# Optimization experiments

Hardware: AMD Instinct MI355X
Metric: run time of the kernel (lower is better)

The kernel has to match this reference:

```python
import jax, jax.numpy as jnp
import numpy as np

B, L, D = 4, 2048, 256
EXPAND, D_STATE, D_CONV = 2, 16, 4
D_INNER = EXPAND * D
DT_RANK = (D + 15) // 16  # ceil(d_model/16) = 16
N_HEADS = 4
H_MLP = int(D * 4.0)
EPS = 1e-5


def _ln(x, w, b):
    mu = x.mean(-1, keepdims=True)
    var = ((x - mu) ** 2).mean(-1, keepdims=True)
    return (x - mu) / jnp.sqrt(var + EPS) * w + b


def _silu(x):
    return x * jax.nn.sigmoid(x)


def _mamba(x, Win, convw, convb, Wx, Wdt, bdt, Alog, Dp, Wout):
    # x: (B, L, D) -> (B, L, D). Standard Mamba mixer (selective scan).
    b, l, d = x.shape
    xz = x @ Win.T                      # (b, l, 2*d_inner)
    xi, z = jnp.split(xz, 2, axis=-1)
    # depthwise causal conv1d, kernel D_CONV
    xc = jnp.swapaxes(xi, 1, 2)         # (b, d_inner, l)
    xc = jax.lax.conv_general_dilated(
        xc, convw, (1,), [(D_CONV - 1, 0)],
        feature_group_count=D_INNER, dimension_numbers=('NCW', 'OIW', 'NCW'))
    xi = _silu(jnp.swapaxes(xc + convb[None, :, None], 1, 2))  # (b, l, d_inner)
    dbl = xi @ Wx.T                     # (b, l, dt_rank + 2*d_state)
    dt = jax.nn.softplus(dbl[..., :DT_RANK] @ Wdt.T + bdt)     # (b, l, d_inner)
    Bm = dbl[..., DT_RANK:DT_RANK + D_STATE]                    # (b, l, n)
    Cm = dbl[..., DT_RANK + D_STATE:]                            # (b, l, n)
    A = -jnp.exp(Alog)                  # (d_inner, n)

    def step(h, ins):
        dt_t, B_t, C_t, u_t = ins       # (b,d_inner),(b,n),(b,n),(b,d_inner)
        h = h * jnp.exp(dt_t[..., None] * A) + dt_t[..., None] * B_t[:, None, :] * u_t[..., None]
        return h, jnp.einsum('bdn,bn->bd', h, C_t)

    xs = tuple(jnp.swapaxes(t, 0, 1) for t in (dt, Bm, Cm, xi))  # time-major
    h0 = jnp.zeros((b, D_INNER, D_STATE), x.dtype)
    _, ys = jax.lax.scan(step, h0, xs)  # ys: (l, b, d_inner)
    y = jnp.swapaxes(ys, 0, 1) + xi * Dp
    return (y * _silu(z)) @ Wout.T


def _attn(x, Wqkv, bqkv, Wo, bo):
    b, l, d = x.shape
    hd = d // N_HEADS
    qkv = x @ Wqkv.T + bqkv
    q, k, v = jnp.split(qkv, 3, axis=-1)
    sh = lambda t: t.reshape(b, l, N_HEADS, hd).transpose(0, 2, 1, 3)
    q, k, v = sh(q), sh(k), sh(v)
    a = jax.nn.softmax(jnp.einsum('bhqd,bhkd->bhqk', q, k) / np.float32(np.sqrt(hd)), axis=-1)
    o = jnp.einsum('bhqk,bhkd->bhqd', a, v).transpose(0, 2, 1, 3).reshape(b, l, d)
    return o @ Wo.T + bo


def setup_inputs() -> dict:
    key = jax.random.key(0)
    ks = iter(jax.random.split(key, 40))
    rn = lambda shape, s=0.02: jax.random.normal(next(ks), shape, jnp.float32) * s
    inp = {'x': jax.random.normal(next(ks), (B, L, D), jnp.float32)}
    for p in ('mf', 'mb'):
        inp[p + '_Win'] = rn((2 * D_INNER, D))
        inp[p + '_convw'] = rn((D_INNER, 1, D_CONV), 0.1)
        inp[p + '_convb'] = jnp.zeros((D_INNER,), jnp.float32)
        inp[p + '_Wx'] = rn((DT_RANK + 2 * D_STATE, D_INNER))
        inp[p + '_Wdt'] = rn((D_INNER, DT_RANK), 0.1)
        inp[p + '_bdt'] = rn((D_INNER,), 0.5)
        inp[p + '_Alog'] = jnp.log(jnp.broadcast_to(jnp.arange(1, D_STATE + 1, dtype=jnp.float32), (D_INNER, D_STATE)))
        inp[p + '_D'] = jnp.ones((D_INNER,), jnp.float32)
        inp[p + '_Wout'] = rn((D, D_INNER))
    for n in ('n1', 'n2', 'n3'):
        inp[n + 'w'] = jnp.ones((D,), jnp.float32)
        inp[n + 'b'] = jnp.zeros((D,), jnp.float32)
    inp['Wqkv'] = rn((3 * D, D))
    inp['bqkv'] = jnp.zeros((3 * D,), jnp.float32)
    inp['Wo'] = rn((D, D))
    inp['bo'] = jnp.zeros((D,), jnp.float32)
    inp['fc1w'] = rn((H_MLP, D))
    inp['fc1b'] = jnp.zeros((H_MLP,), jnp.float32)
    inp['fc2w'] = rn((D, H_MLP))
    inp['fc2b'] = jnp.zeros((D,), jnp.float32)
    return inp


def reference(x, n1w, n1b, n2w, n2b, n3w, n3b,
              mf_Win, mf_convw, mf_convb, mf_Wx, mf_Wdt, mf_bdt, mf_Alog, mf_D, mf_Wout,
              mb_Win, mb_convw, mb_convb, mb_Wx, mb_Wdt, mb_bdt, mb_Alog, mb_D, mb_Wout,
              Wqkv, bqkv, Wo, bo, fc1w, fc1b, fc2w, fc2b):
    # Mamba branch (bidirectional): DropPath is identity at eval
    h = _ln(x, n1w, n1b)
    fwd = _mamba(h, mf_Win, mf_convw, mf_convb, mf_Wx, mf_Wdt, mf_bdt, mf_Alog, mf_D, mf_Wout)
    bwd = jnp.flip(_mamba(jnp.flip(h, 1), mb_Win, mb_convw, mb_convb, mb_Wx, mb_Wdt, mb_bdt, mb_Alog, mb_D, mb_Wout), 1)
    x = x + fwd + bwd
    # Attention branch (full attention since window=None)
    x = x + _attn(_ln(x, n2w, n2b), Wqkv, bqkv, Wo, bo)
    # MLP branch (exact GELU like torch default)
    h = _ln(x, n3w, n3b)
    x = x + (jax.nn.gelu(h @ fc1w.T + fc1b, approximate=False) @ fc2w.T + fc2b)
    return x
```

## Files before the change

kernel.cpp:

```cpp
#include <hip/hip_runtime.h>
#include <hip/hip_bf16.h>
#include <math.h>

#define LL 2048
#define DD 256
#define MTOT 8192
#define DINNER 512
#define CT 32
#define NC 64

typedef __attribute__((ext_vector_type(8))) short short8;
typedef __attribute__((ext_vector_type(4))) float f32x4;

__device__ __forceinline__ float us2f(unsigned short u){
  return __uint_as_float(((unsigned)u) << 16);
}
__device__ __forceinline__ unsigned short f2us(float f){
  __hip_bfloat16 h = __float2bfloat16(f);
  return *(unsigned short*)&h;
}
__device__ __forceinline__ float frcp(float x){
  return __builtin_amdgcn_rcpf(x);
}

__global__ void probe_kernel(const unsigned* __restrict__ alog, int* __restrict__ flag){
  if (threadIdx.x == 0 && blockIdx.x == 0) *flag = (alog[0] != 0u) ? 1 : 0;
}

struct Srcs { const void* p[32]; unsigned off[33]; unsigned foff[32]; };

__global__ __launch_bounds__(256) void cvt_all_kernel(Srcs s, float* __restrict__ dst,
                                                      unsigned short* __restrict__ db,
                                                      const int* __restrict__ flag,
                                                      unsigned total){
  unsigned i = blockIdx.x * 256u + threadIdx.x;
  if (i >= total) return;
  int k = 31;
  while (s.off[k] > i) --k;
  unsigned j = i - s.off[k];
  float v;
  if (*flag) v = us2f(((const unsigned short*)s.p[k])[j]);
  else       v = ((const float*)s.p[k])[j];
  if ((k == 24 && j < 65536u) || (k == 25 && j < 256u)) v *= 0.125f;
  db[i] = f2us(v);
  if (s.foff[k] != 0xFFFFFFFFu) dst[s.foff[k] + j] = v;
}

__global__ __launch_bounds__(256) void cvt_x_kernel(const void* __restrict__ src,
                                                    float* __restrict__ dst,
                                                    const int* __restrict__ flag, unsigned n){
  unsigned i = blockIdx.x * 256u + threadIdx.x;
  if (i >= n) return;
  if (*flag) dst[i] = us2f(((const unsigned short*)src)[i]);
  else       dst[i] = ((const float*)src)[i];
}

__global__ __launch_bounds__(256) void zero_kernel(float* __restrict__ p, unsigned n){
  unsigned i = blockIdx.x * 256u + threadIdx.x;
  if (i < n) p[i] = 0.f;
}

__global__ __launch_bounds__(256) void wdbl_prep_kernel(
    const float* __restrict__ Wx, int dsWx, unsigned short* __restrict__ Wd)
{
  const unsigned g = blockIdx.x * 256u + threadIdx.x;
  const int dir = g >> 15;
  const unsigned idx = g & 32767u;
  const int n = idx >> 9, k = idx & 511;
  float v = (n < 48) ? (Wx + (size_t)dir * dsWx)[(size_t)n * 512 + k] : 0.f;
  Wd[g] = f2us(v);
}

__global__ __launch_bounds__(256) void final_out_kernel(
    const float* __restrict__ xf, void* __restrict__ out,
    const int* __restrict__ flag, unsigned n)
{
  unsigned i = blockIdx.x * 256u + threadIdx.x;
  if (i >= n) return;
  float v = xf[i];
  if (*flag) ((unsigned short*)out)[i] = f2us(v);
  else       ((float*)out)[i] = v;
}

enum { G_BF16=0, G_GELU=1, G_RESID=2 };
__global__ __launch_bounds__(256) void gemm_mfma_kernel(
    const unsigned short* __restrict__ A, int lda, int agap,
    const unsigned short* __restrict__ W, const unsigned short* __restrict__ W2,
    int Kw, int nsplit, int ksplit, int msplit,
    const float* __restrict__ bias,
    unsigned short* __restrict__ Cb, float* __restrict__ resid,
    int N, int K, int kslices, int mode)
{
  __shared__ unsigned short sA[64][40];
  __shared__ unsigned short sW[64][40];
  const int tid = threadIdx.x;
  const int w = tid >> 6, lane = tid & 63, quad = lane >> 4, l16 = lane & 15;
  const int m0 = blockIdx.y << 6, n0 = blockIdx.x << 6;
  const int ks = blockIdx.z;
  const int kper = K / kslices;
  const int srow = tid >> 2, skc = (tid & 3) << 3;
  int wr = n0 + srow;
  const unsigned short* Wbase = W;
  if (msplit && m0 >= msplit) Wbase = W2;
  if (nsplit && wr >= nsplit){ Wbase = W2; wr -= nsplit; }
  f32x4 acc[4] = {};
  for (int k0 = ks * kper; k0 < ks * kper + kper; k0 += 32){
    int ac = k0 + skc;
    if (agap && ac >= 512) ac += 512;
    short8 av = *(const short8*)(A + (size_t)(m0 + srow) * lda + ac);
    int kk = k0 + skc;
    const unsigned short* Wp = Wbase;
    if (ksplit && kk >= ksplit){ Wp = W2; kk -= ksplit; }
    short8 wv = *(const short8*)(Wp + (size_t)wr * Kw + kk);
    __syncthreads();
    *(short8*)&sA[srow][skc] = av;
    *(short8*)&sW[srow][skc] = wv;
    __syncthreads();
    short8 af = *(const short8*)&sA[w * 16 + l16][quad << 3];
    #pragma unroll
    for (int ns = 0; ns < 4; ++ns){
      short8 wf = *(const short8*)&sW[ns * 16 + l16][quad << 3];
      acc[ns] = __builtin_amdgcn_mfma_f32_16x16x32_bf16(af, wf, acc[ns], 0, 0, 0);
    }
  }
  #pragma unroll
  for (int ns = 0; ns < 4; ++ns){
    const int n = n0 + ns * 16 + l16;
    const float bv = (bias && (mode != G_RESID || ks == 0)) ? bias[n] : 0.f;
    #pragma unroll
    for (int r = 0; r < 4; ++r){
      const int m = m0 + w * 16 + quad * 4 + r;
      const size_t off = (size_t)m * N + n;
      float v = acc[ns][r] + bv;
      if (mode == G_BF16) Cb[off] = f2us(v);
      else if (mode == G_GELU) Cb[off] = f2us(0.5f * v * (1.f + erff(v * 0.70710678118f)));
      else atomicAdd(resid + off, v);
    }
  }
}

__global__ __launch_bounds__(256) void gemm128_kernel(
    const unsigned short* __restrict__ A, int lda,
    const unsigned short* __restrict__ W, const unsigned short* __restrict__ W2,
    int Kw, int nsplit, const float* __restrict__ bias,
    unsigned short* __restrict__ Cb, int N, int K, int mode)
{
  __shared__ unsigned short sA[128][40];
  __shared__ unsigned short sW[128][40];
  const int tid = threadIdx.x;
  const int w = tid >> 6, lane = tid & 63, quad = lane >> 4, l16 = lane & 15;
  const int wm = (w >> 1) << 6, wn = (w & 1) << 6;
  const int m0 = blockIdx.y << 7, n0 = blockIdx.x << 7;
  const int srow = tid >> 2, skc = (tid & 3) << 3;
  const unsigned short* wrp0;
  const unsigned short* wrp1;
  {
    int r0 = n0 + srow, r1 = n0 + srow + 64;
    const unsigned short* b0 = W;
    const unsigned short* b1 = W;
    if (nsplit){
      if (r0 >= nsplit){ b0 = W2; r0 -= nsplit; }
      if (r1 >= nsplit){ b1 = W2; r1 -= nsplit; }
    }
    wrp0 = b0 + (size_t)r0 * Kw;
    wrp1 = b1 + (size_t)r1 * Kw;
  }
  const unsigned short* arp0 = A + (size_t)(m0 + srow) * lda;
  const unsigned short* arp1 = A + (size_t)(m0 + srow + 64) * lda;
  f32x4 acc[4][4] = {};
  for (int k0 = 0; k0 < K; k0 += 32){
    short8 av0 = *(const short8*)(arp0 + k0 + skc);
    short8 av1 = *(const short8*)(arp1 + k0 + skc);
    short8 wv0 = *(const short8*)(wrp0 + k0 + skc);
    short8 wv1 = *(const short8*)(wrp1 + k0 + skc);
    __syncthreads();
    *(short8*)&sA[srow][skc] = av0;
    *(short8*)&sA[srow + 64][skc] = av1;
    *(short8*)&sW[srow][skc] = wv0;
    *(short8*)&sW[srow + 64][skc] = wv1;
    __syncthreads();
    short8 af[4], wf[4];
    #pragma unroll
    for (int i = 0; i < 4; ++i){
      af[i] = *(const short8*)&sA[wm + i * 16 + l16][quad << 3];
      wf[i] = *(const short8*)&sW[wn + i * 16 + l16][quad << 3];
    }
    #pragma unroll
    for (int mi = 0; mi < 4; ++mi)
      #pragma unroll
      for (int ni = 0; ni < 4; ++ni)
        acc[mi][ni] = __builtin_amdgcn_mfma_f32_16x16x32_bf16(af[mi], wf[ni], acc[mi][ni], 0, 0, 0);
  }
  #pragma unroll
  for (int ni = 0; ni < 4; ++ni){
    const int n = n0 + wn + ni * 16 + l16;
    const float bv = bias ? bias[n] : 0.f;
    #pragma unroll
    for (int mi = 0; mi < 4; ++mi){
      #pragma unroll
      for (int r = 0; r < 4; ++r){
        const int m = m0 + wm + mi * 16 + quad * 4 + r;
        float v = acc[mi][ni][r] + bv;
        if (mode == G_GELU) v = 0.5f * v * (1.f + erff(v * 0.70710678118f));
        Cb[(size_t)m * N + n] = f2us(v);
      }
    }
  }
}

__global__ __launch_bounds__(256) void ln_kernel(
    const float* __restrict__ xin,
    const float* __restrict__ w, const float* __restrict__ b,
    unsigned short* __restrict__ hout)
{
  const int row = blockIdx.x, tid = threadIdx.x;
  const size_t off = (size_t)row * DD + tid;
  float v = xin[off];
  float s = v, s2 = v * v;
  #pragma unroll
  for (int o = 32; o; o >>= 1){ s += __shfl_xor(s, o); s2 += __shfl_xor(s2, o); }
  __shared__ float ls[4], ls2[4];
  if ((tid & 63) == 0){ ls[tid >> 6] = s; ls2[tid >> 6] = s2; }
  __syncthreads();
  s  = ls[0] + ls[1] + ls[2] + ls[3];
  s2 = ls2[0] + ls2[1] + ls2[2] + ls2[3];
  const float mu  = s * (1.f / DD);
  const float var = s2 * (1.f / DD) - mu * mu;
  const float inv = rsqrtf(var + 1e-5f);
  hout[off] = f2us((v - mu) * inv * w[tid] + b[tid]);
}

__global__ __launch_bounds__(256) void conv_silu_kernel(
    const unsigned short* __restrict__ xzc, const float* __restrict__ convw0, int dsCw,
    const float* __restrict__ convb0, int dsCb, unsigned short* __restrict__ xi)
{
  const unsigned g = blockIdx.x * 256u + threadIdx.x;
  const int c4 = (g & 127) << 2;
  const int t = (g >> 7) & 2047;
  const int b = (g >> 18) & 3;
  const int dir = g >> 20;
  const float* cw = convw0 + (size_t)dir * dsCw;
  float4 acc = *(const float4*)(convb0 + (size_t)dir * dsCb + c4);
  float wv[4][4];
  #pragma unroll
  for (int j = 0; j < 4; ++j) *(float4*)wv[j] = *(const float4*)(cw + (c4 + j) * 4);
  #pragma unroll
  for (int k = 0; k < 4; ++k){
    const int tt = dir ? (t + (3 - k)) : (t - 3 + k);
    if ((unsigned)tt < 2048u){
      ushort4 x = *(const ushort4*)(xzc + ((size_t)(b * 2048 + tt)) * 2048 + dir * 1024 + c4);
      acc.x = fmaf(wv[0][k], us2f(x.x), acc.x);
      acc.y = fmaf(wv[1][k], us2f(x.y), acc.y);
      acc.z = fmaf(wv[2][k], us2f(x.z), acc.z);
      acc.w = fmaf(wv[3][k], us2f(x.w), acc.w);
    }
  }
  ushort4 o;
  o.x = f2us(acc.x * frcp(1.f + __expf(-acc.x)));
  o.y = f2us(acc.y * frcp(1.f + __expf(-acc.y)));
  o.z = f2us(acc.z * frcp(1.f + __expf(-acc.z)));
  o.w = f2us(acc.w * frcp(1.f + __expf(-acc.w)));
  *(ushort4*)(xi + (size_t)dir * 4194304 + ((size_t)(b * 2048 + t)) * 512 + c4) = o;
}

__global__ __launch_bounds__(256) void scan_part1_kernel(
    const unsigned short* __restrict__ xib, int dsXi,
    const float* __restrict__ dblc,
    const float* __restrict__ Alog, int dsAl,
    const float* __restrict__ Wdt0, int dsWdt,
    const float* __restrict__ bdt0, int dsBdt,
    float* __restrict__ dtsum, int dsDts,
    float* __restrict__ hend, int dsHend)
{
  const int bx = blockIdx.x;
  const int dg = bx & 1, c = (bx >> 1) & (NC - 1), b = (bx >> 7) & 3, dir = bx >> 9;
  const int tid = threadIdx.x;
  const int d = dg * 256 + tid;
  const unsigned short* xi_ = xib + (size_t)dir * dsXi;
  const float* Al_ = Alog + (size_t)dir * dsAl;
  __shared__ float sDB[CT][32];
  {
    const int s = tid >> 3, c4 = (tid & 7) << 2;
    const int t = dir ? (LL - 1 - (c * CT + s)) : (c * CT + s);
    *(float4*)&sDB[s][c4] =
      *(const float4*)(dblc + ((size_t)(dir * 8192 + b * LL + t)) * 64 + c4);
  }
  float wdt[16];
  {
    const float* wr = Wdt0 + (size_t)dir * dsWdt + (size_t)d * 16;
    #pragma unroll
    for (int q = 0; q < 4; ++q) *(float4*)&wdt[q * 4] = *(const float4*)(wr + q * 4);
  }
  const float bdtd = (bdt0 + (size_t)dir * dsBdt)[d];
  float A[16];
  #pragma unroll
  for (int n = 0; n < 16; ++n) A[n] = -__expf(Al_[d * 16 + n]);
  const float A1 = A[0];
  bool fast = true;
  #pragma unroll
  for (int n = 0; n < 16; ++n)
    fast = fast && (fabsf(A[n] - A1 * (n + 1)) <= 1e-4f * fabsf(A1 * (n + 1)) + 1e-30f);
  __syncthreads();
  float h[16];
  #pragma unroll
  for (int n = 0; n < 16; ++n) h[n] = 0.f;
  float dts = 0.f;
  #pragma unroll 1
  for (int s = 0; s < CT; ++s){
    const int t = dir ? (LL - 1 - (c * CT + s)) : (c * CT + s);
    const size_t row = (size_t)(b * LL + t);
    const float uv  = us2f(xi_[row * 512 + d]);
    f32x4 dv[4], Bv[4];
    #pragma unroll
    for (int q = 0; q < 4; ++q) dv[q] = *(const f32x4*)&sDB[s][q * 4];
    #pragma unroll
    for (int q = 0; q < 4; ++q) Bv[q] = *(const f32x4*)&sDB[s][16 + q * 4];
    float p0 = 0.f, p1 = 0.f, p2 = 0.f, p3 = 0.f;
    #pragma unroll
    for (int j = 0; j < 4; ++j){
      p0 = fmaf(dv[0][j], wdt[j],      p0);
      p1 = fmaf(dv[1][j], wdt[4 + j],  p1);
      p2 = fmaf(dv[2][j], wdt[8 + j],  p2);
      p3 = fmaf(dv[3][j], wdt[12 + j], p3);
    }
    const float dtpre = bdtd + ((p0 + p1) + (p2 + p3));
    const float dtv = (dtpre > 20.f) ? dtpre : __logf(1.f + __expf(dtpre));
    const float dtu = dtv * uv;
    dts += dtv;
    if (fast){
      const float e1 = __expf(dtv * A1);
      const float e2 = e1 * e1;
      float eo = e1, ev = e2;
      #pragma unroll
      for (int m = 0; m < 8; ++m){
        h[2 * m]     = fmaf(h[2 * m],     eo, dtu * Bv[(2 * m) >> 2][(2 * m) & 3]);
        h[2 * m + 1] = fmaf(h[2 * m + 1], ev, dtu * Bv[(2 * m + 1) >> 2][(2 * m + 1) & 3]);
        eo *= e2; ev *= e2;
      }
    } else {
      #pragma unroll
      for (int n = 0; n < 16; ++n){
        const float e = __expf(dtv * A[n]);
        h[n] = fmaf(h[n], e, dtu * Bv[n >> 2][n & 3]);
      }
    }
  }
  const size_t base = (size_t)dir * dsHend + ((size_t)((b * NC + c) * 512 + d)) * 16;
  #pragma unroll
  for (int q = 0; q < 4; ++q) *(float4*)&hend[base + q * 4] = *(const float4*)&h[q * 4];
  dtsum[(size_t)dir * dsDts + (size_t)(b * NC + c) * 512 + d] = dts;
}

__global__ __launch_bounds__(256) void scan_combine_kernel(
    const float* __restrict__ dtsum, int dsDts,
    float* __restrict__ hend, int dsHend,
    const float* __restrict__ Alog, int dsAl)
{
  const unsigned g = blockIdx.x * 256u + threadIdx.x;
  const int dir = g >> 15;
  const unsigned gg = g & 32767u;
  const int b = gg >> 13, d = (gg >> 4) & 511, n = gg & 15;
  const float A = -__expf((Alog + (size_t)dir * dsAl)[d * 16 + n]);
  const float* dts_ = dtsum + (size_t)dir * dsDts;
  float* he_ = hend + (size_t)dir * dsHend;
  float h = 0.f;
  for (int c = 0; c < NC; ++c){
    const size_t sb = ((size_t)((b * NC + c) * 512 + d)) * 16 + n;
    const float e = __expf(dts_[(size_t)(b * NC + c) * 512 + d] * A);
    const float he = he_[sb];
    he_[sb] = h;
    h = h * e + he;
  }
}

__global__ __launch_bounds__(256) void scan_part2_kernel(
    const unsigned short* __restrict__ xib, int dsXi,
    const float* __restrict__ dblc,
    const unsigned short* __restrict__ zin,
    unsigned short* __restrict__ yout,
    const float* __restrict__ Alog, int dsAl,
    const float* __restrict__ Wdt0, int dsWdt,
    const float* __restrict__ bdt0, int dsBdt,
    const float* __restrict__ Dp, int dsD,
    const float* __restrict__ hin, int dsHend)
{
  const int bx = blockIdx.x;
  const int dg = bx & 1, c = (bx >> 1) & (NC - 1), b = (bx >> 7) & 3, dir = bx >> 9;
  const int tid = threadIdx.x;
  const int d = dg * 256 + tid;
  const unsigned short* xi_ = xib + (size_t)dir * dsXi;
  const unsigned short* z_ = zin + dir * 1024;
  unsigned short* y_ = yout + dir * 1024;
  const float* Al_ = Alog + (size_t)dir * dsAl;
  __shared__ float sDB[CT][48];
  for (int i4 = tid; i4 < 384; i4 += 256){
    const int s = i4 / 12, cc = (i4 - s * 12) << 2;
    const int t = dir ? (LL - 1 - (c * CT + s)) : (c * CT + s);
    *(float4*)&sDB[s][cc] =
      *(const float4*)(dblc + ((size_t)(dir * 8192 + b * LL + t)) * 64 + cc);
  }
  float wdt[16];
  {
    const float* wr = Wdt0 + (size_t)dir * dsWdt + (size_t)d * 16;
    #pragma unroll
    for (int q = 0; q < 4; ++q) *(float4*)&wdt[q * 4] = *(const float4*)(wr + q * 4);
  }
  const float bdtd = (bdt0 + (size_t)dir * dsBdt)[d];
  float A[16];
  #pragma unroll
  for (int n = 0; n < 16; ++n) A[n] = -__expf(Al_[d * 16 + n]);
  const float A1 = A[0];
  bool fast = true;
  #pragma unroll
  for (int n = 0; n < 16; ++n)
    fast = fast && (fabsf(A[n] - A1 * (n + 1)) <= 1e-4f * fabsf(A1 * (n + 1)) + 1e-30f);
  const float Dv = (Dp + (size_t)dir * dsD)[d];
  __syncthreads();
  float h[16];
  const size_t base = (size_t)dir * dsHend + ((size_t)((b * NC + c) * 512 + d)) * 16;
  #pragma unroll
  for (int q = 0; q < 4; ++q) *(float4*)&h[q * 4] = *(const float4*)&hin[base + q * 4];
  #pragma unroll 1
  for (int s = 0; s < CT; ++s){
    const int t = dir ? (LL - 1 - (c * CT + s)) : (c * CT + s);
    const size_t row = (size_t)(b * LL + t);
    const float uv = us2f(xi_[row * 512 + d]);
    const float z  = us2f(z_[row * 2048 + d]);
    f32x4 dv[4];
    #pragma unroll
    for (int q = 0; q < 4; ++q) dv[q] = *(const f32x4*)&sDB[s][q * 4];
    float p0 = 0.f, p1 = 0.f, p2 = 0.f, p3 = 0.f;
    #pragma unroll
    for (int j = 0; j < 4; ++j){
      p0 = fmaf(dv[0][j], wdt[j],      p0);
      p1 = fmaf(dv[1][j], wdt[4 + j],  p1);
      p2 = fmaf(dv[2][j], wdt[8 + j],  p2);
      p3 = fmaf(dv[3][j], wdt[12 + j], p3);
    }
    const float dtpre = bdtd + ((p0 + p1) + (p2 + p3));
    const float dtv = (dtpre > 20.f) ? dtpre : __logf(1.f + __expf(dtpre));
    const float dtu = dtv * uv;
    f32x4 Bv[4], Cv[4];
    #pragma unroll
    for (int q = 0; q < 4; ++q) Bv[q] = *(const f32x4*)&sDB[s][16 + q * 4];
    #pragma unroll
    for (int q = 0; q < 4; ++q) Cv[q] = *(const f32x4*)&sDB[s][32 + q * 4];
    float pA = uv * Dv, pB = 0.f;
    if (fast){
      const float e1 = __expf(dtv * A1);
      const float e2 = e1 * e1;
      float eo = e1, ev = e2;
      #pragma unroll
      for (int m = 0; m < 8; ++m){
        const int n0 = 2 * m, n1 = 2 * m + 1;
        h[n0] = fmaf(h[n0], eo, dtu * Bv[n0 >> 2][n0 & 3]);
        pA = fmaf(h[n0], Cv[n0 >> 2][n0 & 3], pA);
        h[n1] = fmaf(h[n1], ev, dtu * Bv[n1 >> 2][n1 & 3]);
        pB = fmaf(h[n1], Cv[n1 >> 2][n1 & 3], pB);
        eo *= e2; ev *= e2;
      }
    } else {
      #pragma unroll
      for (int n = 0; n < 16; ++n){
        const float e = __expf(dtv * A[n]);
        h[n] = fmaf(h[n], e, dtu * Bv[n >> 2][n & 3]);
        pA = fmaf(h[n], Cv[n >> 2][n & 3], pA);
      }
    }
    const float p = pA + pB;
    const float sig = frcp(1.f + __expf(-z));
    y_[row * 2048 + d] = f2us(p * z * sig);
  }
}

__global__ __launch_bounds__(256) void v_prep_kernel(
    const unsigned short* __restrict__ qkvb, unsigned short* __restrict__ Vt)
{
  const int kt = blockIdx.x;
  const int bh = blockIdx.y;
  const int b = bh >> 2, h = bh & 3;
  __shared__ unsigned short tile[64][72];
  #pragma unroll
  for (int rr = 0; rr < 4; ++rr){
    const int idx = (rr * 256 + threadIdx.x) * 4;
    const int key = idx >> 6, d = idx & 63;
    ushort4 v = *(const ushort4*)(qkvb + ((size_t)(b * 2048 + kt * 64 + key)) * 768 + 512 + h * 64 + d);
    *(ushort4*)&tile[key][d] = v;
  }
  __syncthreads();
  #pragma unroll
  for (int rr = 0; rr < 8; ++rr){
    const int o2 = rr * 256 + threadIdx.x;
    const int d = o2 >> 5, k2 = (o2 & 31) << 1;
    ushort2 u;
    u.x = tile[k2][d];
    u.y = tile[k2 + 1][d];
    *(ushort2*)(Vt + (size_t)bh * 131072 + (size_t)d * 2048 + kt * 64 + k2) = u;
  }
}

__global__ __launch_bounds__(256) void attn_mfma_kernel(
    const unsigned short* __restrict__ qkvb, const unsigned short* __restrict__ Vt,
    float* __restrict__ op0, float* __restrict__ op1, float* __restrict__ lpart)
{
  __shared__ unsigned short sK[64][72];
  __shared__ unsigned short sV[64][72];
  __shared__ unsigned short sP[4][32][68];
  const int tid = threadIdx.x;
  const int w = tid >> 6, lane = tid & 63, quad = lane >> 4, l16 = lane & 15;
  const int bh = blockIdx.y;
  const int b = bh >> 2, h = bh & 3;
  const int q0 = blockIdx.x * 128;
  const int split = blockIdx.z;

  short8 qf[2][2];
  #pragma unroll
  for (int qs = 0; qs < 2; ++qs){
    const unsigned short* qp = qkvb + ((size_t)(b * 2048 + q0 + w * 32 + qs * 16 + l16)) * 768 + h * 64 + quad * 8;
    qf[qs][0] = *(const short8*)qp;
    qf[qs][1] = *(const short8*)(qp + 32);
  }

  f32x4 o[2][4] = {};
  float lsum[2][4] = {};

  const int kt0 = split * 512;
  for (int kt = kt0; kt < kt0 + 512; kt += 64){
    __syncthreads();
    #pragma unroll
    for (int r = 0; r < 2; ++r){
      const int idx = (r * 256 + tid) * 8;
      const int row = idx >> 6, c = idx & 63;
      *(short8*)&sK[row][c] = *(const short8*)(qkvb + ((size_t)(b * 2048 + kt + row)) * 768 + 256 + h * 64 + c);
      *(short8*)&sV[row][c] = *(const short8*)(Vt + (size_t)bh * 131072 + (size_t)row * 2048 + kt + c);
    }
    __syncthreads();

    #pragma unroll
    for (int qs = 0; qs < 2; ++qs){
      float p[4][4];
      #pragma unroll
      for (int sub = 0; sub < 4; ++sub){
        short8 bk0 = *(const short8*)&sK[sub * 16 + l16][quad * 8];
        short8 bk1 = *(const short8*)&sK[sub * 16 + l16][32 + quad * 8];
        f32x4 acc = {0,0,0,0};
        acc = __builtin_amdgcn_mfma_f32_16x16x32_bf16(qf[qs][0], bk0, acc, 0, 0, 0);
        acc = __builtin_amdgcn_mfma_f32_16x16x32_bf16(qf[qs][1], bk1, acc, 0, 0, 0);
        #pragma unroll
        for (int r = 0; r < 4; ++r) p[sub][r] = __expf(acc[r]);
      }
      #pragma unroll
      for (int r = 0; r < 4; ++r)
        lsum[qs][r] += p[0][r] + p[1][r] + p[2][r] + p[3][r];
      #pragma unroll
      for (int sub = 0; sub < 4; ++sub)
        #pragma unroll
        for (int r = 0; r < 4; ++r)
          sP[w][qs * 16 + quad * 4 + r][sub * 16 + l16] = f2us(p[sub][r]);
    }
    __builtin_amdgcn_s_waitcnt(0);
    #pragma unroll
    for (int qs = 0; qs < 2; ++qs){
      short8 pa0 = *(const short8*)&sP[w][qs * 16 + l16][quad * 8];
      short8 pa1 = *(const short8*)&sP[w][qs * 16 + l16][32 + quad * 8];
      #pragma unroll
      for (int nsub = 0; nsub < 4; ++nsub){
        short8 bv0 = *(const short8*)&sV[nsub * 16 + l16][quad * 8];
        short8 bv1 = *(const short8*)&sV[nsub * 16 + l16][32 + quad * 8];
        o[qs][nsub] = __builtin_amdgcn_mfma_f32_16x16x32_bf16(pa0, bv0, o[qs][nsub], 0, 0, 0);
        o[qs][nsub] = __builtin_amdgcn_mfma_f32_16x16x32_bf16(pa1, bv1, o[qs][nsub], 0, 0, 0);
      }
    }
  }

  float* op = (split < 2 ? op0 : op1) + (size_t)(split & 1) * 2097152;
  #pragma unroll
  for (int qs = 0; qs < 2; ++qs){
    #pragma unroll
    for (int r = 0; r < 4; ++r){
      float l = lsum[qs][r];
      l += __shfl_xor(l, 1); l += __shfl_xor(l, 2);
      l += __shfl_xor(l, 4); l += __shfl_xor(l, 8);
      const int q = q0 + w * 32 + qs * 16 + quad * 4 + r;
      #pragma unroll
      for (int nsub = 0; nsub < 4; ++nsub)
        op[((size_t)bh * 2048 + q) * 64 + nsub * 16 + l16] = o[qs][nsub][r];
      if (l16 == 0) lpart[(split * 16 + bh) * 2048 + q] = l;
    }
  }
}

__global__ __launch_bounds__(256) void attn_merge_kernel(
    const float* __restrict__ op0, const float* __restrict__ op1,
    const float* __restrict__ lpart, unsigned short* __restrict__ outp)
{
  const unsigned g = blockIdx.x * 256u + threadIdx.x;
  const int d4 = (g & 15) << 2;
  const int q = (g >> 4) & 2047;
  const int bh = g >> 15;
  float4 s = make_float4(0.f, 0.f, 0.f, 0.f);
  float l = 0.f;
  #pragma unroll
  for (int sp = 0; sp < 4; ++sp){
    const float* op = (sp < 2 ? op0 : op1) + (size_t)(sp & 1) * 2097152;
    float4 o = *(const float4*)(op + ((size_t)bh * 2048 + q) * 64 + d4);
    s.x += o.x; s.y += o.y; s.z += o.z; s.w += o.w;
    l += lpart[(sp * 16 + bh) * 2048 + q];
  }
  const float invl = 1.f / l;
  const int b = bh >> 2, h = bh & 3;
  ushort4 u;
  u.x = f2us(s.x * invl);
  u.y = f2us(s.y * invl);
  u.z = f2us(s.z * invl);
  u.w = f2us(s.w * invl);
  *(ushort4*)(outp + ((size_t)(b * 2048 + q)) * 256 + h * 64 + d4) = u;
}

extern "C" void kernel_launch(void* const* d_in, const int* in_sizes, int n_in,
                              void* d_out, int out_size, void* d_ws, size_t ws_size,
                              hipStream_t stream)
{
  static const bool needf[33] = {
    false, false,true,true,true,true,true,true,true,false,
    false,true,true,true,true,true,true,true,false,
    true,true,true,true,true,true,
    false,true,false,true,false,true,false,true };

  int* flag  = (int*)d_ws;
  float* wts = (float*)d_ws + 16;

  Srcs srcs;
  unsigned acc = 0, facc = 0;
  unsigned foff_h[33];
  for (int i = 1; i <= 32; ++i){
    srcs.p[i - 1] = d_in[i];
    srcs.off[i - 1] = acc;
    acc += (unsigned)in_sizes[i];
    if (needf[i]){ srcs.foff[i - 1] = facc; foff_h[i] = facc; facc += (unsigned)in_sizes[i]; }
    else { srcs.foff[i - 1] = 0xFFFFFFFFu; foff_h[i] = 0xFFFFFFFFu; }
  }
  srcs.off[32] = acc;
  const unsigned wtotal = acc;
  const unsigned ftot = (facc + 3u) & ~3u;

  unsigned short* wb16 = (unsigned short*)(wts + ftot);
  float* xf    = wts + ftot + (wtotal + 1) / 2;
  float* xzc_f = xf + 2097152;
  float* xi_f  = xzc_f + 8388608;
  float* dblc  = xi_f + 4194304;
  float* hb_f  = dblc + 1048576;
  float* hend  = hb_f + 1048576;
  float* dtsum = hend + 4194304;
  float* wd_f  = dtsum + 262144;

  unsigned short* xzc  = (unsigned short*)xzc_f;
  unsigned short* xi16 = (unsigned short*)xi_f;
  unsigned short* hb16 = (unsigned short*)hb_f;
  unsigned short* wdbl = (unsigned short*)wd_f;
  unsigned short* qkvb = xzc;
  unsigned short* Vt   = (unsigned short*)hend;
  float* op0   = xzc_f + 4194304;
  float* op1   = xi_f;
  float* lpart = dtsum;
  unsigned short* fc1o = xzc;

  auto wp  = [&](int i){ return wts + foff_h[i]; };
  auto wp16= [&](int i){ return wb16 + srcs.off[i - 1]; };

  hipLaunchKernelGGL(probe_kernel, dim3(1), dim3(64), 0, stream,
      (const unsigned*)d_in[7], flag);
  hipLaunchKernelGGL(cvt_all_kernel, dim3((wtotal + 255) / 256), dim3(256), 0, stream,
      srcs, wts, wb16, flag, wtotal);
  hipLaunchKernelGGL(cvt_x_kernel, dim3(MTOT * DD / 256), dim3(256), 0, stream,
      d_in[0], xf, flag, (unsigned)(MTOT * DD));

  const int dsCw = (int)(foff_h[11] - foff_h[2]);
  const int dsAl = (int)(foff_h[16] - foff_h[7]);
  const int dsD  = (int)(foff_h[17] - foff_h[8]);
  const int dsWx = (int)(foff_h[13] - foff_h[4]);
  const int dsWdt= (int)(foff_h[14] - foff_h[5]);
  const int dsBdt= (int)(foff_h[15] - foff_h[6]);
  const int dsCb2= (int)(foff_h[12] - foff_h[3]);

  hipLaunchKernelGGL(wdbl_prep_kernel, dim3(256), dim3(256), 0, stream,
      wp(4), dsWx, wdbl);

  auto gemm16 = [&](const unsigned short* Ab, int lda, int agap, int M,
                    const unsigned short* W, const unsigned short* W2,
                    int Kw, int nsplit, int ksplit, int msplit, const float* bias,
                    unsigned short* Cb, float* resid,
                    int N, int K, int ksl, int mode){
    hipLaunchKernelGGL(gemm_mfma_kernel, dim3(N / 64, M / 64, ksl), dim3(256), 0, stream,
        Ab, lda, agap, W, W2, Kw, nsplit, ksplit, msplit, bias, Cb, resid, N, K, ksl, mode);
  };
  auto gemm128 = [&](const unsigned short* Ab, int lda, int M,
                     const unsigned short* W, const unsigned short* W2,
                     int Kw, int nsplit, const float* bias,
                     unsigned short* Cb, int N, int K, int mode){
    hipLaunchKernelGGL(gemm128_kernel, dim3(N / 128, M / 128), dim3(256), 0, stream,
        Ab, lda, W, W2, Kw, nsplit, bias, Cb, N, K, mode);
  };

  hipLaunchKernelGGL(ln_kernel, dim3(MTOT), dim3(256), 0, stream,
      xf, wp(19), wp(20), hb16);

  gemm128(hb16, 256, MTOT, wp16(1), wp16(10), 256, 1024, nullptr,
          xzc, 2048, 256, G_BF16);
  hipLaunchKernelGGL(conv_silu_kernel, dim3(8192), dim3(256), 0, stream,
      xzc, wp(2), dsCw, wp(3), dsCb2, xi16);
  hipLaunchKernelGGL(zero_kernel, dim3(4096), dim3(256), 0, stream, dblc, 1048576u);
  gemm16(xi16, 512, 0, 2 * MTOT, wdbl, wdbl + 32768, 512, 0, 0, MTOT, nullptr,
         nullptr, dblc, 64, 512, 4, G_RESID);
  hipLaunchKernelGGL(scan_part1_kernel, dim3(1024), dim3(256), 0, stream,
      xi16, 4194304, dblc, wp(7), dsAl, wp(5), dsWdt, wp(6), dsBdt,
      dtsum, 131072, hend, 2097152);
  hipLaunchKernelGGL(scan_combine_kernel, dim3(256), dim3(256), 0, stream,
      dtsum, 131072, hend, 2097152, wp(7), dsAl);
  hipLaunchKernelGGL(scan_part2_kernel, dim3(1024), dim3(256), 0, stream,
      xi16, 4194304, dblc, xzc + 512, xzc, wp(7), dsAl, wp(5), dsWdt, wp(6), dsBdt,
      wp(8), dsD, hend, 2097152);
  gemm16(xzc, 2048, 1, MTOT, wp16(9), wp16(18), 512, 0, 512, 0, nullptr,
         nullptr, xf, 256, 1024, 2, G_RESID);

  hipLaunchKernelGGL(ln_kernel, dim3(MTOT), dim3(256), 0, stream,
      xf, wp(21), wp(22), hb16);
  gemm128(hb16, 256, MTOT, wp16(25), nullptr, 256, 0, wp(26),
          qkvb, 768, 256, G_BF16);
  hipLaunchKernelGGL(v_prep_kernel, dim3(32, 16), dim3(256), 0, stream,
      qkvb, Vt);
  hipLaunchKernelGGL(attn_mfma_kernel, dim3(16, 16, 4), dim3(256), 0, stream,
      qkvb, Vt, op0, op1, lpart);
  hipLaunchKernelGGL(attn_merge_kernel, dim3(2048), dim3(256), 0, stream,
      op0, op1, lpart, hb16);
  gemm16(hb16, 256, 0, MTOT, wp16(27), nullptr, 256, 0, 0, 0, wp(28),
         nullptr, xf, 256, 256, 2, G_RESID);

  hipLaunchKernelGGL(ln_kernel, dim3(MTOT), dim3(256), 0, stream,
      xf, wp(23), wp(24), hb16);
  gemm128(hb16, 256, MTOT, wp16(29), nullptr, 256, 0, wp(30),
          fc1o, 1024, 256, G_GELU);
  gemm16(fc1o, 1024, 0, MTOT, wp16(31), nullptr, 1024, 0, 0, 0, nullptr,
         nullptr, xf, 256, 1024, 2, G_RESID);
  hipLaunchKernelGGL(final_out_kernel, dim3(MTOT * DD / 256), dim3(256), 0, stream,
      xf, d_out, flag, (unsigned)(MTOT * DD));
}
```

Baseline: 455.9 us.

## Drop split-K atomics in GEMMs and stage scan inputs in shared memory

The 64-tile GEMMs drop split-K (kslices set to 1) and replace atomicAdd with a plain read-add-write into the residual, or a direct store for the x_proj output via a new G_STF mode. This removes the separate zeroing kernel for the dbl buffer. Both scan kernels now preload each chunk's xi (and z) rows into shared memory with coalesced 16-byte loads instead of doing a strided 2-byte global load per timestep. The trade-off is fewer blocks, and so less parallelism, for the small-N GEMMs with large K.

```diff
diff --git a/kernel.cpp b/kernel.cpp
--- a/kernel.cpp
+++ b/kernel.cpp
@@ -55,11 +55,6 @@
   else       dst[i] = ((const float*)src)[i];
 }
 
-__global__ __launch_bounds__(256) void zero_kernel(float* __restrict__ p, unsigned n){
-  unsigned i = blockIdx.x * 256u + threadIdx.x;
-  if (i < n) p[i] = 0.f;
-}
-
 __global__ __launch_bounds__(256) void wdbl_prep_kernel(
     const float* __restrict__ Wx, int dsWx, unsigned short* __restrict__ Wd)
 {
@@ -82,7 +77,7 @@
   else       ((float*)out)[i] = v;
 }
 
-enum { G_BF16=0, G_GELU=1, G_RESID=2 };
+enum { G_BF16=0, G_GELU=1, G_RESID=2, G_STF=3 };
 __global__ __launch_bounds__(256) void gemm_mfma_kernel(
     const unsigned short* __restrict__ A, int lda, int agap,
     const unsigned short* __restrict__ W, const unsigned short* __restrict__ W2,
@@ -126,7 +121,7 @@
   #pragma unroll
   for (int ns = 0; ns < 4; ++ns){
     const int n = n0 + ns * 16 + l16;
-    const float bv = (bias && (mode != G_RESID || ks == 0)) ? bias[n] : 0.f;
+    const float bv = (bias && ks == 0) ? bias[n] : 0.f;
     #pragma unroll
     for (int r = 0; r < 4; ++r){
       const int m = m0 + w * 16 + quad * 4 + r;
@@ -134,7 +129,8 @@
       float v = acc[ns][r] + bv;
       if (mode == G_BF16) Cb[off] = f2us(v);
       else if (mode == G_GELU) Cb[off] = f2us(0.5f * v * (1.f + erff(v * 0.70710678118f)));
-      else atomicAdd(resid + off, v);
+      else if (mode == G_RESID) resid[off] += v;
+      else resid[off] = v;
     }
   }
 }
@@ -279,12 +275,21 @@
   const unsigned short* xi_ = xib + (size_t)dir * dsXi;
   const float* Al_ = Alog + (size_t)dir * dsAl;
   __shared__ float sDB[CT][32];
+  __shared__ unsigned short sXI[CT][256];
   {
     const int s = tid >> 3, c4 = (tid & 7) << 2;
     const int t = dir ? (LL - 1 - (c * CT + s)) : (c * CT + s);
     *(float4*)&sDB[s][c4] =
       *(const float4*)(dblc + ((size_t)(dir * 8192 + b * LL + t)) * 64 + c4);
   }
+  #pragma unroll
+  for (int p = 0; p < 4; ++p){
+    const int s = p * 8 + (tid >> 5);
+    const int dc = (tid & 31) << 3;
+    const int t = dir ? (LL - 1 - (c * CT + s)) : (c * CT + s);
+    *(short8*)&sXI[s][dc] =
+      *(const short8*)(xi_ + ((size_t)(b * LL + t)) * 512 + dg * 256 + dc);
+  }
   float wdt[16];
   {
     const float* wr = Wdt0 + (size_t)dir * dsWdt + (size_t)d * 16;
@@ -307,9 +312,7 @@
   float dts = 0.f;
   #pragma unroll 1
   for (int s = 0; s < CT; ++s){
-    const int t = dir ? (LL - 1 - (c * CT + s)) : (c * CT + s);
-    const size_t row = (size_t)(b * LL + t);
-    const float uv  = us2f(xi_[row * 512 + d]);
+    const float uv = us2f(sXI[s][tid]);
     f32x4 dv[4], Bv[4];
     #pragma unroll
     for (int q = 0; q < 4; ++q) dv[q] = *(const f32x4*)&sDB[s][q * 4];
@@ -393,11 +396,22 @@
   unsigned short* y_ = yout + dir * 1024;
   const float* Al_ = Alog + (size_t)dir * dsAl;
   __shared__ float sDB[CT][48];
+  __shared__ unsigned short sXI[CT][256];
+  __shared__ unsigned short sZ[CT][256];
   for (int i4 = tid; i4 < 384; i4 += 256){
     const int s = i4 / 12, cc = (i4 - s * 12) << 2;
     const int t = dir ? (LL - 1 - (c * CT + s)) : (c * CT + s);
     *(float4*)&sDB[s][cc] =
       *(const float4*)(dblc + ((size_t)(dir * 8192 + b * LL + t)) * 64 + cc);
+  }
+  #pragma unroll
+  for (int p = 0; p < 4; ++p){
+    const int s = p * 8 + (tid >> 5);
+    const int dc = (tid & 31) << 3;
+    const int t = dir ? (LL - 1 - (c * CT + s)) : (c * CT + s);
+    const size_t row = (size_t)(b * LL + t);
+    *(short8*)&sXI[s][dc] = *(const short8*)(xi_ + row * 512 + dg * 256 + dc);
+    *(short8*)&sZ[s][dc]  = *(const short8*)(z_ + row * 2048 + dg * 256 + dc);
   }
   float wdt[16];
   {
@@ -424,8 +438,8 @@
   for (int s = 0; s < CT; ++s){
     const int t = dir ? (LL - 1 - (c * CT + s)) : (c * CT + s);
     const size_t row = (size_t)(b * LL + t);
-    const float uv = us2f(xi_[row * 512 + d]);
-    const float z  = us2f(z_[row * 2048 + d]);
+    const float uv = us2f(sXI[s][tid]);
+    const float z  = us2f(sZ[s][tid]);
     f32x4 dv[4];
     #pragma unroll
     for (int q = 0; q < 4; ++q) dv[q] = *(const f32x4*)&sDB[s][q * 4];
@@ -709,9 +723,8 @@
           xzc, 2048, 256, G_BF16);
   hipLaunchKernelGGL(conv_silu_kernel, dim3(8192), dim3(256), 0, stream,
       xzc, wp(2), dsCw, wp(3), dsCb2, xi16);
-  hipLaunchKernelGGL(zero_kernel, dim3(4096), dim3(256), 0, stream, dblc, 1048576u);
   gemm16(xi16, 512, 0, 2 * MTOT, wdbl, wdbl + 32768, 512, 0, 0, MTOT, nullptr,
-         nullptr, dblc, 64, 512, 4, G_RESID);
+         nullptr, dblc, 64, 512, 1, G_STF);
   hipLaunchKernelGGL(scan_part1_kernel, dim3(1024), dim3(256), 0, stream,
       xi16, 4194304, dblc, wp(7), dsAl, wp(5), dsWdt, wp(6), dsBdt,
       dtsum, 131072, hend, 2097152);
@@ -721,7 +734,7 @@
       xi16, 4194304, dblc, xzc + 512, xzc, wp(7), dsAl, wp(5), dsWdt, wp(6), dsBdt,
       wp(8), dsD, hend, 2097152);
   gemm16(xzc, 2048, 1, MTOT, wp16(9), wp16(18), 512, 0, 512, 0, nullptr,
-         nullptr, xf, 256, 1024, 2, G_RESID);
+         nullptr, xf, 256, 1024, 1, G_RESID);
 
   hipLaunchKernelGGL(ln_kernel, dim3(MTOT), dim3(256), 0, stream,
       xf, wp(21), wp(22), hb16);
@@ -734,14 +747,14 @@
   hipLaunchKernelGGL(attn_merge_kernel, dim3(2048), dim3(256), 0, stream,
       op0, op1, lpart, hb16);
   gemm16(hb16, 256, 0, MTOT, wp16(27), nullptr, 256, 0, 0, 0, wp(28),
-         nullptr, xf, 256, 256, 2, G_RESID);
+         nullptr, xf, 256, 256, 1, G_RESID);
 
   hipLaunchKernelGGL(ln_kernel, dim3(MTOT), dim3(256), 0, stream,
       xf, wp(23), wp(24), hb16);
   gemm128(hb16, 256, MTOT, wp16(29), nullptr, 256, 0, wp(30),
           fc1o, 1024, 256, G_GELU);
   gemm16(fc1o, 1024, 0, MTOT, wp16(31), nullptr, 1024, 0, 0, 0, nullptr,
-         nullptr, xf, 256, 1024, 2, G_RESID);
+         nullptr, xf, 256, 1024, 1, G_RESID);
   hipLaunchKernelGGL(final_out_kernel, dim3(MTOT * DD / 256), dim3(256), 0, stream,
       xf, d_out, flag, (unsigned)(MTOT * DD));
 }
```

Result: faster. 439.9 us (-3.5%).
